# Kernel tuning notes

Measured on AMD Instinct MI355X. Metric: run time of the kernel, lower is better.

The kernel has to match this reference:

```python
import jax, jax.numpy as jnp
import numpy as np

B = 4194304
RAD2DEG = 180.0 / np.pi


def setup_inputs() -> dict:
    key = jax.random.key(0)
    k1, k2, k3 = jax.random.split(key, 3)
    label = jax.random.normal(k1, (B, 3, 2), dtype=jnp.float32)
    est_label = jax.random.normal(k2, (B, 6), dtype=jnp.float32)
    mix_way = jax.random.randint(k3, (B,), 0, 2, dtype=jnp.int32)  # 0='single', 1=mixed
    return {"label": label, "est_label": est_label, "mix_way": mix_way}


def reference(label, est_label, mix_way):
    # --- permutation-invariant MSE loss ---
    e1, e2 = est_label[:, :3], est_label[:, 3:]            # [B,3] each
    l1, l2 = label[:, :, 0], label[:, :, 1]                 # [B,3] each
    mse = lambda a, b: jnp.mean((a - b) ** 2, axis=-1)      # per-batch mean over 3 comps
    loss_perm1 = mse(e1, l1) + mse(e2, l2)                  # [B]
    loss_perm2 = mse(e2, l1) + mse(e1, l2)                  # [B]
    mixed_loss = jnp.minimum(loss_perm1, loss_perm2)        # [B]
    # 'single' branch in the original uses the FULL (unindexed) tensors -> same scalar each time
    single_loss = jnp.mean((est_label[:, :3] - label[:, :, 0]) ** 2)
    per_batch = jnp.where(mix_way == 0, single_loss, mixed_loss)
    label_loss = jnp.mean(per_batch)

    # --- azimuth MAE with angle wrap-around and best pairing ---
    lab_az1 = jnp.arctan2(label[:, 1, 0], label[:, 0, 0]) * RAD2DEG
    lab_az2 = jnp.arctan2(label[:, 1, 1], label[:, 0, 1]) * RAD2DEG
    est_az1 = jnp.arctan2(est_label[:, 1], est_label[:, 0]) * RAD2DEG
    est_az2 = jnp.arctan2(est_label[:, 4], est_label[:, 3]) * RAD2DEG

    def wrap(e):
        e = jnp.abs(e)
        return jnp.where(e > 180.0, 360.0 - e, e)

    e11 = wrap(lab_az1 - est_az1)
    e22 = wrap(lab_az2 - est_az2)
    e12 = wrap(lab_az1 - est_az2)
    e21 = wrap(lab_az2 - est_az1)

    use_direct = (e11 + e22) < (e12 + e21)
    mae1 = jnp.mean(jnp.where(use_direct, e11, e12))
    mae2 = jnp.mean(jnp.where(use_direct, e22, e21))

    return (label_loss, mae1, mae2)
```

## Files before the change

### kernel.cpp

```cpp
#include <hip/hip_runtime.h>
#include <math.h>

#define RAD2DEG 57.29577951308232f

constexpr int S1_BLOCKS = 2048;
constexpr int S1_TPB    = 256;

__device__ __forceinline__ float angdist_deg(float ax, float ay,
                                             float bx, float by) {
    float dot = ax * bx + ay * by;
    float cr  = fabsf(ay * bx - ax * by);
    float ad  = fabsf(dot);
    float mn  = fminf(cr, ad);
    float mx  = fmaxf(cr, ad);
    float t   = mn * __builtin_amdgcn_rcpf(fmaxf(mx, 1e-37f));
    float s   = t * t;
    float p = fmaf(s, -0.01172120f, 0.05265332f);
    p = fmaf(s, p, -0.11643287f);
    p = fmaf(s, p,  0.19354346f);
    p = fmaf(s, p, -0.33262347f);
    p = fmaf(s, p,  0.99997726f);
    float a = t * p;
    a = (cr > ad)    ? (1.57079632679489662f - a) : a;
    a = (dot < 0.0f) ? (3.14159265358979323f - a) : a;
    return a * RAD2DEG;
}

__device__ __forceinline__ void per_row(
    float l1x, float l2x, float l1y, float l2y, float l1z, float l2z,
    float e1x, float e1y, float e1z, float e2x, float e2y, float e2z,
    int mw,
    float& sS, float& sM, float& sC0, float& sM1, float& sM2)
{
    float dx, dy, dz;
    dx = e1x - l1x; dy = e1y - l1y; dz = e1z - l1z;
    float d11 = dx*dx + dy*dy + dz*dz;
    dx = e2x - l2x; dy = e2y - l2y; dz = e2z - l2z;
    float d22 = dx*dx + dy*dy + dz*dz;
    dx = e2x - l1x; dy = e2y - l1y; dz = e2z - l1z;
    float d21 = dx*dx + dy*dy + dz*dz;
    dx = e1x - l2x; dy = e1y - l2y; dz = e1z - l2z;
    float d12 = dx*dx + dy*dy + dz*dz;

    sS += d11;

    float mixed = fminf(d11 + d22, d21 + d12) * (1.0f / 3.0f);
    float m = (mw != 0) ? 1.0f : 0.0f;
    sM  += m * mixed;
    sC0 += 1.0f - m;

    float e11 = angdist_deg(l1x, l1y, e1x, e1y);
    float e22 = angdist_deg(l2x, l2y, e2x, e2y);
    float e12 = angdist_deg(l1x, l1y, e2x, e2y);
    float e21 = angdist_deg(l2x, l2y, e1x, e1y);

    bool ud = (e11 + e22) < (e12 + e21);
    sM1 += ud ? e11 : e12;
    sM2 += ud ? e22 : e21;
}

__global__ __launch_bounds__(S1_TPB) void stage1_kernel(
    const float* __restrict__ label,
    const float* __restrict__ est,
    const int*   __restrict__ mix,
    float* __restrict__ partials,
    int P)
{
    const int tid = threadIdx.x;
    const int gid = blockIdx.x * S1_TPB + tid;
    const int T   = gridDim.x * S1_TPB;

    float sS = 0.f, sM = 0.f, sC0 = 0.f, sM1 = 0.f, sM2 = 0.f;

    for (int p = gid; p < P; p += T) {
        const float4* lab4 = (const float4*)(label + (size_t)p * 12);
        const float4* est4 = (const float4*)(est   + (size_t)p * 12);
        float4 L0 = lab4[0], L1 = lab4[1], L2 = lab4[2];
        float4 E0 = est4[0], E1 = est4[1], E2 = est4[2];
        int2 mw = ((const int2*)mix)[p];

        per_row(L0.x, L0.y, L0.z, L0.w, L1.x, L1.y,
                E0.x, E0.y, E0.z, E0.w, E1.x, E1.y,
                mw.x, sS, sM, sC0, sM1, sM2);
        per_row(L1.z, L1.w, L2.x, L2.y, L2.z, L2.w,
                E1.z, E1.w, E2.x, E2.y, E2.z, E2.w,
                mw.y, sS, sM, sC0, sM1, sM2);
    }

    for (int off = 32; off > 0; off >>= 1) {
        sS  += __shfl_down(sS,  off, 64);
        sM  += __shfl_down(sM,  off, 64);
        sC0 += __shfl_down(sC0, off, 64);
        sM1 += __shfl_down(sM1, off, 64);
        sM2 += __shfl_down(sM2, off, 64);
    }

    __shared__ float red[S1_TPB / 64][5];
    const int wid = tid >> 6, lane = tid & 63;
    if (lane == 0) {
        red[wid][0] = sS; red[wid][1] = sM; red[wid][2] = sC0;
        red[wid][3] = sM1; red[wid][4] = sM2;
    }
    __syncthreads();
    if (tid == 0) {
        float r0 = 0.f, r1 = 0.f, r2 = 0.f, r3 = 0.f, r4 = 0.f;
        #pragma unroll
        for (int w = 0; w < S1_TPB / 64; ++w) {
            r0 += red[w][0]; r1 += red[w][1]; r2 += red[w][2];
            r3 += red[w][3]; r4 += red[w][4];
        }
        float* out = partials + (size_t)blockIdx.x * 5;
        out[0] = r0; out[1] = r1; out[2] = r2; out[3] = r3; out[4] = r4;
    }
}

__global__ __launch_bounds__(256) void stage2_kernel(
    const float* __restrict__ partials,
    float* __restrict__ out,
    int nblocks,
    long long Btot)
{
    const int tid = threadIdx.x;
    double aS = 0, aM = 0, aC0 = 0, aM1 = 0, aM2 = 0;
    for (int r = tid; r < nblocks; r += 256) {
        const float* row = partials + (size_t)r * 5;
        aS += row[0]; aM += row[1]; aC0 += row[2]; aM1 += row[3]; aM2 += row[4];
    }
    for (int off = 32; off > 0; off >>= 1) {
        aS  += __shfl_down(aS,  off, 64);
        aM  += __shfl_down(aM,  off, 64);
        aC0 += __shfl_down(aC0, off, 64);
        aM1 += __shfl_down(aM1, off, 64);
        aM2 += __shfl_down(aM2, off, 64);
    }
    __shared__ double red[4][5];
    const int wid = tid >> 6, lane = tid & 63;
    if (lane == 0) {
        red[wid][0] = aS; red[wid][1] = aM; red[wid][2] = aC0;
        red[wid][3] = aM1; red[wid][4] = aM2;
    }
    __syncthreads();
    if (tid == 0) {
        double S = 0, M = 0, C0 = 0, M1 = 0, M2 = 0;
        #pragma unroll
        for (int w = 0; w < 4; ++w) {
            S += red[w][0]; M += red[w][1]; C0 += red[w][2];
            M1 += red[w][3]; M2 += red[w][4];
        }
        const double Bd = (double)Btot;
        const double single_loss = S / (3.0 * Bd);
        out[0] = (float)((C0 * single_loss + M) / Bd);
        out[1] = (float)(M1 / Bd);
        out[2] = (float)(M2 / Bd);
    }
}

extern "C" void kernel_launch(void* const* d_in, const int* in_sizes, int n_in,
                              void* d_out, int out_size, void* d_ws, size_t ws_size,
                              hipStream_t stream) {
    const float* label = (const float*)d_in[0];
    const float* est   = (const float*)d_in[1];
    const int*   mix   = (const int*)d_in[2];
    float* out = (float*)d_out;
    float* partials = (float*)d_ws;

    const long long B = (long long)in_sizes[2];
    const int P = (int)(B / 2);

    stage1_kernel<<<S1_BLOCKS, S1_TPB, 0, stream>>>(label, est, mix, partials, P);
    stage2_kernel<<<1, 256, 0, stream>>>(partials, out, S1_BLOCKS, B);
}
```

Before: 231.7 us.

## Stage label/est loads through LDS via global_load_lds for coalesced access

Replaces per-thread strided float4 loads of 48-byte rows with cooperative, fully coalesced 16-byte global-to-LDS direct loads of 256-pair chunks, then each thread reads its row from shared memory. The intent is better coalescing of the input stream in this memory-bound reduction. It adds two block barriers per chunk, which serialise loading and compute within a block, plus 24 KB of LDS per block that can limit occupancy. A scalar tail loop handles leftover pairs.

```diff
diff --git a/kernel.cpp b/kernel.cpp
--- a/kernel.cpp
+++ b/kernel.cpp
@@ -5,6 +5,16 @@
 
 constexpr int S1_BLOCKS = 2048;
 constexpr int S1_TPB    = 256;
+constexpr int CHUNK     = 256;
+constexpr int CH_F      = CHUNK * 12;
+constexpr int CH_V4     = CHUNK * 3;
+
+typedef __attribute__((address_space(1))) const unsigned int gu32;
+typedef __attribute__((address_space(3))) unsigned int       lu32;
+
+__device__ __forceinline__ void g2lds16(const float4* g, float* lds) {
+    __builtin_amdgcn_global_load_lds((gu32*)g, (lu32*)lds, 16, 0, 0);
+}
 
 __device__ __forceinline__ float angdist_deg(float ax, float ay,
                                              float bx, float by) {
@@ -66,18 +76,35 @@
     float* __restrict__ partials,
     int P)
 {
-    const int tid = threadIdx.x;
-    const int gid = blockIdx.x * S1_TPB + tid;
-    const int T   = gridDim.x * S1_TPB;
+    __shared__ float labS[CH_F];
+    __shared__ float estS[CH_F];
+
+    const int tid  = threadIdx.x;
+    const int wid  = tid >> 6;
+    const int lane = tid & 63;
+
+    const float4* lab4 = (const float4*)label;
+    const float4* est4 = (const float4*)est;
+    const int2*   mix2 = (const int2*)mix;
 
     float sS = 0.f, sM = 0.f, sC0 = 0.f, sM1 = 0.f, sM2 = 0.f;
 
-    for (int p = gid; p < P; p += T) {
-        const float4* lab4 = (const float4*)(label + (size_t)p * 12);
-        const float4* est4 = (const float4*)(est   + (size_t)p * 12);
-        float4 L0 = lab4[0], L1 = lab4[1], L2 = lab4[2];
-        float4 E0 = est4[0], E1 = est4[1], E2 = est4[2];
-        int2 mw = ((const int2*)mix)[p];
+    const int nchunks = P / CHUNK;
+    for (int c = blockIdx.x; c < nchunks; c += gridDim.x) {
+        const int vbase = c * CH_V4;
+        #pragma unroll
+        for (int j = 0; j < 3; ++j) {
+            const int vi = j * 256 + wid * 64;
+            g2lds16(lab4 + vbase + vi + lane, labS + vi * 4);
+            g2lds16(est4 + vbase + vi + lane, estS + vi * 4);
+        }
+        int2 mw = mix2[c * CHUNK + tid];
+        __syncthreads();
+
+        const float4* Lv = (const float4*)(labS + tid * 12);
+        const float4* Ev = (const float4*)(estS + tid * 12);
+        float4 L0 = Lv[0], L1 = Lv[1], L2 = Lv[2];
+        float4 E0 = Ev[0], E1 = Ev[1], E2 = Ev[2];
 
         per_row(L0.x, L0.y, L0.z, L0.w, L1.x, L1.y,
                 E0.x, E0.y, E0.z, E0.w, E1.x, E1.y,
@@ -85,6 +112,22 @@
         per_row(L1.z, L1.w, L2.x, L2.y, L2.z, L2.w,
                 E1.z, E1.w, E2.x, E2.y, E2.z, E2.w,
                 mw.y, sS, sM, sC0, sM1, sM2);
+        __syncthreads();
+    }
+
+    for (int p = nchunks * CHUNK + blockIdx.x * S1_TPB + tid; p < P;
+         p += gridDim.x * S1_TPB) {
+        const float4* lv = (const float4*)(label + (size_t)p * 12);
+        const float4* ev = (const float4*)(est   + (size_t)p * 12);
+        float4 L0 = lv[0], L1 = lv[1], L2 = lv[2];
+        float4 E0 = ev[0], E1 = ev[1], E2 = ev[2];
+        int2 mw = mix2[p];
+        per_row(L0.x, L0.y, L0.z, L0.w, L1.x, L1.y,
+                E0.x, E0.y, E0.z, E0.w, E1.x, E1.y,
+                mw.x, sS, sM, sC0, sM1, sM2);
+        per_row(L1.z, L1.w, L2.x, L2.y, L2.z, L2.w,
+                E1.z, E1.w, E2.x, E2.y, E2.z, E2.w,
+                mw.y, sS, sM, sC0, sM1, sM2);
     }
 
     for (int off = 32; off > 0; off >>= 1) {
@@ -96,7 +139,6 @@
     }
 
     __shared__ float red[S1_TPB / 64][5];
-    const int wid = tid >> 6, lane = tid & 63;
     if (lane == 0) {
         red[wid][0] = sS; red[wid][1] = sM; red[wid][2] = sC0;
         red[wid][3] = sM1; red[wid][4] = sM2;
```

New measurement: 229.7 us. Within noise of the previous version (-0.9%).

## Use contiguous per-block chunks with 2x unrolled loads and double grid size

Applied to the files above, without the earlier changes.

Each block now handles one contiguous chunk of row pairs instead of a grid-stride slice. The loop is unrolled so each thread issues loads for two pairs before computing, which puts more memory requests in flight. The grid grows from 2048 to 4096 blocks, and indices are widened to 64-bit. The aim is better latency hiding and DRAM locality on a bandwidth-bound reduction, at the cost of more registers and a larger partials buffer.

```diff
diff --git a/kernel.cpp b/kernel.cpp
--- a/kernel.cpp
+++ b/kernel.cpp
@@ -3,7 +3,7 @@
 
 #define RAD2DEG 57.29577951308232f
 
-constexpr int S1_BLOCKS = 2048;
+constexpr int S1_BLOCKS = 4096;
 constexpr int S1_TPB    = 256;
 
 __device__ __forceinline__ float angdist_deg(float ax, float ay,
@@ -59,32 +59,71 @@
     sM2 += ud ? e22 : e21;
 }
 
+__device__ __forceinline__ void do_pair(
+    const float4* __restrict__ lab4, const float4* __restrict__ est4,
+    const int2* __restrict__ mix2, long long p,
+    float& sS, float& sM, float& sC0, float& sM1, float& sM2)
+{
+    const float4* lv = lab4 + p * 3;
+    const float4* ev = est4 + p * 3;
+    float4 L0 = lv[0], L1 = lv[1], L2 = lv[2];
+    float4 E0 = ev[0], E1 = ev[1], E2 = ev[2];
+    int2 mw = mix2[p];
+    per_row(L0.x, L0.y, L0.z, L0.w, L1.x, L1.y,
+            E0.x, E0.y, E0.z, E0.w, E1.x, E1.y,
+            mw.x, sS, sM, sC0, sM1, sM2);
+    per_row(L1.z, L1.w, L2.x, L2.y, L2.z, L2.w,
+            E1.z, E1.w, E2.x, E2.y, E2.z, E2.w,
+            mw.y, sS, sM, sC0, sM1, sM2);
+}
+
 __global__ __launch_bounds__(S1_TPB) void stage1_kernel(
     const float* __restrict__ label,
     const float* __restrict__ est,
     const int*   __restrict__ mix,
     float* __restrict__ partials,
-    int P)
+    long long P)
 {
     const int tid = threadIdx.x;
-    const int gid = blockIdx.x * S1_TPB + tid;
-    const int T   = gridDim.x * S1_TPB;
+    const long long ppb   = (P + gridDim.x - 1) / gridDim.x;
+    const long long start = (long long)blockIdx.x * ppb;
+    const long long end   = (start + ppb < P) ? (start + ppb) : P;
+
+    const float4* lab4 = (const float4*)label;
+    const float4* est4 = (const float4*)est;
+    const int2*   mix2 = (const int2*)mix;
 
     float sS = 0.f, sM = 0.f, sC0 = 0.f, sM1 = 0.f, sM2 = 0.f;
 
-    for (int p = gid; p < P; p += T) {
-        const float4* lab4 = (const float4*)(label + (size_t)p * 12);
-        const float4* est4 = (const float4*)(est   + (size_t)p * 12);
-        float4 L0 = lab4[0], L1 = lab4[1], L2 = lab4[2];
-        float4 E0 = est4[0], E1 = est4[1], E2 = est4[2];
-        int2 mw = ((const int2*)mix)[p];
-
-        per_row(L0.x, L0.y, L0.z, L0.w, L1.x, L1.y,
-                E0.x, E0.y, E0.z, E0.w, E1.x, E1.y,
-                mw.x, sS, sM, sC0, sM1, sM2);
-        per_row(L1.z, L1.w, L2.x, L2.y, L2.z, L2.w,
-                E1.z, E1.w, E2.x, E2.y, E2.z, E2.w,
-                mw.y, sS, sM, sC0, sM1, sM2);
+    for (long long p0 = start + tid; p0 < end; p0 += 2 * S1_TPB) {
+        const long long p1 = p0 + S1_TPB;
+        if (p1 < end) {
+            const float4* lv0 = lab4 + p0 * 3;
+            const float4* ev0 = est4 + p0 * 3;
+            const float4* lv1 = lab4 + p1 * 3;
+            const float4* ev1 = est4 + p1 * 3;
+            float4 A0 = lv0[0], A1 = lv0[1], A2 = lv0[2];
+            float4 B0 = ev0[0], B1 = ev0[1], B2 = ev0[2];
+            float4 C0 = lv1[0], C1 = lv1[1], C2 = lv1[2];
+            float4 D0 = ev1[0], D1 = ev1[1], D2 = ev1[2];
+            int2 mwa = mix2[p0];
+            int2 mwb = mix2[p1];
+
+            per_row(A0.x, A0.y, A0.z, A0.w, A1.x, A1.y,
+                    B0.x, B0.y, B0.z, B0.w, B1.x, B1.y,
+                    mwa.x, sS, sM, sC0, sM1, sM2);
+            per_row(A1.z, A1.w, A2.x, A2.y, A2.z, A2.w,
+                    B1.z, B1.w, B2.x, B2.y, B2.z, B2.w,
+                    mwa.y, sS, sM, sC0, sM1, sM2);
+            per_row(C0.x, C0.y, C0.z, C0.w, C1.x, C1.y,
+                    D0.x, D0.y, D0.z, D0.w, D1.x, D1.y,
+                    mwb.x, sS, sM, sC0, sM1, sM2);
+            per_row(C1.z, C1.w, C2.x, C2.y, C2.z, C2.w,
+                    D1.z, D1.w, D2.x, D2.y, D2.z, D2.w,
+                    mwb.y, sS, sM, sC0, sM1, sM2);
+        } else {
+            do_pair(lab4, est4, mix2, p0, sS, sM, sC0, sM1, sM2);
+        }
     }
 
     for (int off = 32; off > 0; off >>= 1) {
@@ -165,7 +204,7 @@
     float* partials = (float*)d_ws;
 
     const long long B = (long long)in_sizes[2];
-    const int P = (int)(B / 2);
+    const long long P = B / 2;
 
     stage1_kernel<<<S1_BLOCKS, S1_TPB, 0, stream>>>(label, est, mix, partials, P);
     stage2_kernel<<<1, 256, 0, stream>>>(partials, out, S1_BLOCKS, B);
```

Measured after the change: 231.7 us. Within noise of the previous version (-0.0%).

## Use contiguous per-block chunks with XCD remap and register double-buffered loads

Applied to the files above, without the earlier changes.

Each block now processes one contiguous range of row pairs instead of a grid-stride interleave. Block indices are remapped so that consecutive chunks land on the same XCD, which is meant to improve L2 locality. The loop software-prefetches the next pair's loads into registers while computing the current pair, and launch bounds request 4 blocks per CU. The prefetch raises register pressure, and the remap assumes the grid size is a multiple of 8.

```diff
diff --git a/kernel.cpp b/kernel.cpp
--- a/kernel.cpp
+++ b/kernel.cpp
@@ -59,32 +59,69 @@
     sM2 += ud ? e22 : e21;
 }
 
-__global__ __launch_bounds__(S1_TPB) void stage1_kernel(
+struct PairData {
+    float4 L0, L1, L2, E0, E1, E2;
+    int2   mw;
+};
+
+__device__ __forceinline__ PairData load_pair(
+    const float4* __restrict__ lab4, const float4* __restrict__ est4,
+    const int2* __restrict__ mix2, long long p)
+{
+    PairData d;
+    const float4* lv = lab4 + p * 3;
+    const float4* ev = est4 + p * 3;
+    d.L0 = lv[0]; d.L1 = lv[1]; d.L2 = lv[2];
+    d.E0 = ev[0]; d.E1 = ev[1]; d.E2 = ev[2];
+    d.mw = mix2[p];
+    return d;
+}
+
+__device__ __forceinline__ void compute_pair(
+    const PairData& d,
+    float& sS, float& sM, float& sC0, float& sM1, float& sM2)
+{
+    per_row(d.L0.x, d.L0.y, d.L0.z, d.L0.w, d.L1.x, d.L1.y,
+            d.E0.x, d.E0.y, d.E0.z, d.E0.w, d.E1.x, d.E1.y,
+            d.mw.x, sS, sM, sC0, sM1, sM2);
+    per_row(d.L1.z, d.L1.w, d.L2.x, d.L2.y, d.L2.z, d.L2.w,
+            d.E1.z, d.E1.w, d.E2.x, d.E2.y, d.E2.z, d.E2.w,
+            d.mw.y, sS, sM, sC0, sM1, sM2);
+}
+
+__global__ __launch_bounds__(S1_TPB, 4) void stage1_kernel(
     const float* __restrict__ label,
     const float* __restrict__ est,
     const int*   __restrict__ mix,
     float* __restrict__ partials,
-    int P)
+    long long P)
 {
     const int tid = threadIdx.x;
-    const int gid = blockIdx.x * S1_TPB + tid;
-    const int T   = gridDim.x * S1_TPB;
+
+    const int nb   = gridDim.x;
+    const int xcd  = blockIdx.x & 7;
+    const int slot = blockIdx.x >> 3;
+    const int b    = xcd * (nb >> 3) + slot;
+
+    const long long ppb   = (P + nb - 1) / nb;
+    const long long start = (long long)b * ppb;
+    const long long end   = (start + ppb < P) ? (start + ppb) : P;
+
+    const float4* lab4 = (const float4*)label;
+    const float4* est4 = (const float4*)est;
+    const int2*   mix2 = (const int2*)mix;
 
     float sS = 0.f, sM = 0.f, sC0 = 0.f, sM1 = 0.f, sM2 = 0.f;
 
-    for (int p = gid; p < P; p += T) {
-        const float4* lab4 = (const float4*)(label + (size_t)p * 12);
-        const float4* est4 = (const float4*)(est   + (size_t)p * 12);
-        float4 L0 = lab4[0], L1 = lab4[1], L2 = lab4[2];
-        float4 E0 = est4[0], E1 = est4[1], E2 = est4[2];
-        int2 mw = ((const int2*)mix)[p];
-
-        per_row(L0.x, L0.y, L0.z, L0.w, L1.x, L1.y,
-                E0.x, E0.y, E0.z, E0.w, E1.x, E1.y,
-                mw.x, sS, sM, sC0, sM1, sM2);
-        per_row(L1.z, L1.w, L2.x, L2.y, L2.z, L2.w,
-                E1.z, E1.w, E2.x, E2.y, E2.z, E2.w,
-                mw.y, sS, sM, sC0, sM1, sM2);
+    long long p = start + tid;
+    if (p < end) {
+        PairData cur = load_pair(lab4, est4, mix2, p);
+        for (; p + S1_TPB < end; p += S1_TPB) {
+            PairData nxt = load_pair(lab4, est4, mix2, p + S1_TPB);
+            compute_pair(cur, sS, sM, sC0, sM1, sM2);
+            cur = nxt;
+        }
+        compute_pair(cur, sS, sM, sC0, sM1, sM2);
     }
 
     for (int off = 32; off > 0; off >>= 1) {
@@ -109,7 +146,7 @@
             r0 += red[w][0]; r1 += red[w][1]; r2 += red[w][2];
             r3 += red[w][3]; r4 += red[w][4];
         }
-        float* out = partials + (size_t)blockIdx.x * 5;
+        float* out = partials + (size_t)b * 5;
         out[0] = r0; out[1] = r1; out[2] = r2; out[3] = r3; out[4] = r4;
     }
 }
@@ -165,7 +202,7 @@
     float* partials = (float*)d_ws;
 
     const long long B = (long long)in_sizes[2];
-    const int P = (int)(B / 2);
+    const long long P = B / 2;
 
     stage1_kernel<<<S1_BLOCKS, S1_TPB, 0, stream>>>(label, est, mix, partials, P);
     stage2_kernel<<<1, 256, 0, stream>>>(partials, out, S1_BLOCKS, B);
```

Measured after the change: 237.6 us. +2.5%, slower.
